# Kernel tuning notes

Measured on AMD Instinct MI355X. Metric: run time of the kernel, lower is better.

Reference implementation:

```python
import jax, jax.numpy as jnp
import numpy as np

N, L, V, IN_DIM, H, E = 128, 128, 8000, 64, 13, 2048
G = 4 * H  # LSTM gate dim (52)

def _lstm_scan(xs, Wih, Whh, b, h0, c0):
    # xs: [L, N, D]; returns final (h, c), each [N, H]
    def step(carry, x_t):
        h, c = carry
        g = x_t @ Wih.T + h @ Whh.T + b
        i, f, gg, o = jnp.split(g, 4, axis=-1)
        c = jax.nn.sigmoid(f) * c + jax.nn.sigmoid(i) * jnp.tanh(gg)
        h = jax.nn.sigmoid(o) * jnp.tanh(c)
        return (h, c), None
    (h, c), _ = jax.lax.scan(step, (h0, c0), xs)
    return h, c

def _gcn_layer(x, W, b, src, dst, norm):
    # GCNConv: out[t] = sum_{(s,t)} norm_st * (x W)[s] + b  (self loops included in src/dst)
    msg = (x @ W)[src] * norm[:, None]
    return jax.ops.segment_sum(msg, dst, num_segments=N) + b

def _gnn(x, params, src, dst, norm):
    W1, b1, W2, b2, Wf, bf = params
    x = jax.nn.leaky_relu(_gcn_layer(x, W1, b1, src, dst, norm), 0.01)
    x = jax.nn.leaky_relu(_gcn_layer(x, W2, b2, src, dst, norm), 0.01)
    return x @ Wf + bf

def setup_inputs():
    ks = iter(jax.random.split(jax.random.key(0), 64))
    def rn(*shape):
        return jax.random.normal(next(ks), shape, dtype=jnp.float32) * 0.1
    inp = {}
    inp["x_tokens"] = jax.random.randint(next(ks), (N, L), 0, V, dtype=jnp.int32)
    inp["edge_index"] = jax.random.randint(next(ks), (2, E), 0, N, dtype=jnp.int32)
    inp["emb"] = rn(V + 1, IN_DIM).at[V].set(0.0)  # padding_idx row zeroed
    for d in ("f", "b"):
        inp["Wih_%s_enc" % d] = rn(G, IN_DIM)
        inp["Whh_%s_enc" % d] = rn(G, H)
        inp["b_%s_enc" % d] = rn(G)
    inp["Wp1"] = rn(2 * H, 2 * H); inp["bp1"] = rn(2 * H)
    inp["Wp2"] = rn(2 * H, 2 * H); inp["bp2"] = rn(2 * H)
    for g in ("gh", "gc"):
        inp[g + "_W1"] = rn(2 * H, 16); inp[g + "_b1"] = rn(16)
        inp[g + "_W2"] = rn(16, 32);    inp[g + "_b2"] = rn(32)
        inp[g + "_Wf"] = rn(32, 2 * H); inp[g + "_bf"] = rn(2 * H)
    for d in ("f", "b"):
        inp["Wih_%s_dec" % d] = rn(G, 1)
        inp["Whh_%s_dec" % d] = rn(G, H)
        inp["b_%s_dec" % d] = rn(G)
    inp["Wout"] = rn(V, 2 * H); inp["bout"] = rn(V)
    return inp

def reference(x_tokens, edge_index, emb, Wih_f_enc, Whh_f_enc, b_f_enc, Wih_b_enc, Whh_b_enc, b_b_enc, Wp1, bp1, Wp2, bp2, gh_W1, gh_b1, gh_W2, gh_b2, gh_Wf, gh_bf, gc_W1, gc_b1, gc_W2, gc_b2, gc_Wf, gc_bf, Wih_f_dec, Whh_f_dec, b_f_dec, Wih_b_dec, Whh_b_dec, b_b_dec, Wout, bout):
    # --- per-node biLSTM encode ---
    xs = jnp.swapaxes(emb[x_tokens], 0, 1)          # [L, N, IN_DIM]
    z = jnp.zeros((N, H), jnp.float32)
    hf, cf = _lstm_scan(xs, Wih_f_enc, Whh_f_enc, b_f_enc, z, z)
    hb, cb = _lstm_scan(xs[::-1], Wih_b_enc, Whh_b_enc, b_b_enc, z, z)
    state_h = jnp.concatenate([hf, hb], -1) @ Wp1.T + bp1   # [N, 2H]
    state_c = jnp.concatenate([cf, cb], -1) @ Wp2.T + bp2
    # --- GCN fusion (symmetric norm with self loops) ---
    ar = jnp.arange(N, dtype=edge_index.dtype)
    src = jnp.concatenate([edge_index[0], ar])
    dst = jnp.concatenate([edge_index[1], ar])
    deg = jax.ops.segment_sum(jnp.ones_like(src, jnp.float32), dst, num_segments=N)
    dinv = jax.lax.rsqrt(jnp.maximum(deg, 1.0))
    norm = dinv[src] * dinv[dst]
    sh = _gnn(state_h, (gh_W1, gh_b1, gh_W2, gh_b2, gh_Wf, gh_bf), src, dst, norm).reshape(N, 2, H)
    sc = _gnn(state_c, (gc_W1, gc_b1, gc_W2, gc_b2, gc_Wf, gc_bf), src, dst, norm).reshape(N, 2, H)
    # --- decoder: each step is a single-timestep biLSTM; original code only
    # passes the GNN state at step 0 and uses a fresh ZERO state for i>0 ---
    prev = jnp.concatenate([jnp.full((N, 1), -1.0, jnp.float32), x_tokens[:, :-1].astype(jnp.float32)], axis=1)  # [N, L]
    first = (jnp.arange(L) == 0)[None, :, None]
    def dec_cell(h0, c0, Wih, Whh, b):
        g = prev[..., None] * Wih[:, 0] + jnp.einsum('nlh,gh->nlg', h0, Whh) + b
        i, f, gg, o = jnp.split(g, 4, axis=-1)
        c = jax.nn.sigmoid(f) * c0 + jax.nn.sigmoid(i) * jnp.tanh(gg)
        return jax.nn.sigmoid(o) * jnp.tanh(c)
    h_f = dec_cell(jnp.where(first, sh[:, 0][:, None, :], 0.0), jnp.where(first, sc[:, 0][:, None, :], 0.0), Wih_f_dec, Whh_f_dec, b_f_dec)
    h_b = dec_cell(jnp.where(first, sh[:, 1][:, None, :], 0.0), jnp.where(first, sc[:, 1][:, None, :], 0.0), Wih_b_dec, Whh_b_dec, b_b_dec)
    dec_out = jnp.concatenate([h_f, h_b], -1)       # [N, L, 2H]
    return jnp.einsum('nld,vd->nlv', dec_out, Wout) + bout   # [N, L, V]
```

## Files before the change

### kernel.cpp

```cpp
#include <hip/hip_runtime.h>
#include <stdint.h>

#define N_    128
#define L_    128
#define V_    8000
#define IN_   64
#define H_    13
#define G_    52
#define E_    2048
#define TWOH  26
#define TOTW  742808

typedef unsigned int   u32;
typedef unsigned short u16;

__device__ __forceinline__ float bfu(u16 u){
    u32 x = ((u32)u) << 16; float f; __builtin_memcpy(&f, &x, 4); return f;
}
__device__ __forceinline__ float sigf(float x){
    x = fminf(fmaxf(x, -30.f), 30.f);
    return 1.0f / (1.0f + __expf(-x));
}
__device__ __forceinline__ float tanh_(float x){
    x = fminf(fmaxf(x, -15.f), 15.f);
    float e = __expf(2.0f * x); return 1.0f - 2.0f / (e + 1.0f);
}

__global__ __launch_bounds__(64) void k_detect(const u16* __restrict__ emb_u16,
                                               int* __restrict__ flag){
    const int lane = threadIdx.x;
    int wild = 0;
    for (int i = lane; i < 1024; i += 64){
        u16 u = emb_u16[i];
        int e = (u >> 7) & 0xFF;
        int tame = (u == 0) || (u == 0x8000) || (e >= 0x60 && e <= 0x88);
        wild += !tame;
    }
    #pragma unroll
    for (int o = 32; o; o >>= 1) wild += __shfl_down(wild, o, 64);
    if (lane == 0) *flag = (wild > 200) ? 1 : 0;
}

struct P31 { const void* p[31]; };

__global__ __launch_bounds__(256) void k_convert(P31 a, const int* __restrict__ flag,
                                                 float* __restrict__ cw){
    const int fp32 = *flag;
    const int i = blockIdx.x * 256 + threadIdx.x;
    if (i >= TOTW) return;
    const int offs[32] = {
        0, 512064, 515392, 516068, 516120, 519448, 520124, 520176, 520852,
        520878, 521554, 521580, 521996, 522012, 522524, 522556, 523388,
        523414, 523830, 523846, 524358, 524390, 525222, 525248, 525300,
        525976, 526028, 526080, 526756, 526808, 734808, TOTW };
    int seg = 0;
    while (i >= offs[seg + 1]) ++seg;
    const int k = i - offs[seg];
    cw[i] = fp32 ? ((const float*)a.p[seg])[k] : bfu(((const u16*)a.p[seg])[k]);
}

__global__ __launch_bounds__(128) void k_proj(const float* __restrict__ emb,
                                              const float* __restrict__ WihF,
                                              const float* __restrict__ WihB,
                                              float* __restrict__ projF,
                                              float* __restrict__ projB){
    __shared__ float x[IN_];
    const int t = blockIdx.x;
    const int tid = threadIdx.x;
    if (tid < IN_) x[tid] = emb[t * IN_ + tid];
    __syncthreads();
    if (tid < 2 * G_){
        const int dir = tid / G_;
        const int g   = tid - dir * G_;
        const float* w = (dir ? WihB : WihF) + g * IN_;
        float acc = 0.f;
        #pragma unroll
        for (int i = 0; i < IN_; ++i) acc += x[i] * w[i];
        (dir ? projB : projF)[t * G_ + g] = acc;
    }
}

__global__ __launch_bounds__(128) void k_lstm(const int* __restrict__ toks_g,
        const float* __restrict__ projF, const float* __restrict__ projB,
        const float* __restrict__ WhhF, const float* __restrict__ bF,
        const float* __restrict__ WhhB, const float* __restrict__ bB,
        const float* __restrict__ Wp1, const float* __restrict__ bp1,
        const float* __restrict__ Wp2, const float* __restrict__ bp2,
        float* __restrict__ state_h, float* __restrict__ state_c){
    __shared__ int   toks[L_];
    __shared__ float hcat[TWOH];
    __shared__ float ccat[TWOH];
    const int n = blockIdx.x, tid = threadIdx.x;
    const int wave = tid >> 6, lane = tid & 63;
    if (tid < L_) toks[tid] = toks_g[n * L_ + tid];

    const float* proj = wave ? projB : projF;
    const float* Whh  = wave ? WhhB : WhhF;
    const float* bp   = wave ? bB   : bF;

    float wh[H_];
    #pragma unroll
    for (int j = 0; j < H_; ++j) wh[j] = 0.f;
    float bb = 0.f;
    if (lane < G_){
        bb = bp[lane];
        #pragma unroll
        for (int j = 0; j < H_; ++j) wh[j] = Whh[lane * H_ + j];
    }
    __syncthreads();

    float h = 0.f, c = 0.f;
    int tok0 = wave ? toks[L_ - 1] : toks[0];
    float gpre = (lane < G_) ? proj[tok0 * G_ + lane] : 0.f;

    for (int t = 0; t < L_; ++t){
        float gv = gpre + bb;
        if (t + 1 < L_){
            int tn = wave ? toks[L_ - 2 - t] : toks[t + 1];
            gpre = (lane < G_) ? proj[tn * G_ + lane] : 0.f;
        }
        #pragma unroll
        for (int j = 0; j < H_; ++j) gv += __shfl(h, j, 64) * wh[j];
        float iv = __shfl(gv, lane,      64);
        float fv = __shfl(gv, lane + 13, 64);
        float gg = __shfl(gv, lane + 26, 64);
        float ov = __shfl(gv, lane + 39, 64);
        c = sigf(fv) * c + sigf(iv) * tanh_(gg);
        h = sigf(ov) * tanh_(c);
    }

    if (lane < H_){ hcat[wave * H_ + lane] = h; ccat[wave * H_ + lane] = c; }
    __syncthreads();

    if (lane < TWOH){
        if (wave == 0){
            float a = bp1[lane];
            #pragma unroll
            for (int k = 0; k < TWOH; ++k) a += hcat[k] * Wp1[lane * TWOH + k];
            state_h[n * TWOH + lane] = a;
        } else {
            float a = bp2[lane];
            #pragma unroll
            for (int k = 0; k < TWOH; ++k) a += ccat[k] * Wp2[lane * TWOH + k];
            state_c[n * TWOH + lane] = a;
        }
    }
}

__global__ __launch_bounds__(256) void k_gcn(const int* __restrict__ eidx,
        const float* __restrict__ state_h, const float* __restrict__ state_c,
        const float* gh_W1, const float* gh_b1, const float* gh_W2, const float* gh_b2,
        const float* gh_Wf, const float* gh_bf,
        const float* gc_W1, const float* gc_b1, const float* gc_W2, const float* gc_b2,
        const float* gc_Wf, const float* gc_bf,
        float* __restrict__ sh, float* __restrict__ sc){
    __shared__ float xs[N_][33];
    __shared__ float xw[N_][33];
    __shared__ float dinv[N_];
    __shared__ int   ptr[N_ + 1];
    __shared__ int   cnt[N_];
    __shared__ int   scn[N_];
    __shared__ int   srcs[E_];
    const int tid = threadIdx.x;
    const int p = blockIdx.x;
    const float* xin = p ? state_c : state_h;
    const float* W1  = p ? gc_W1 : gh_W1;  const float* b1  = p ? gc_b1 : gh_b1;
    const float* W2  = p ? gc_W2 : gh_W2;  const float* b2  = p ? gc_b2 : gh_b2;
    const float* Wf  = p ? gc_Wf : gh_Wf;  const float* bfp = p ? gc_bf : gh_bf;
    float* outp = p ? sc : sh;

    for (int i = tid; i < N_ * TWOH; i += 256) xs[i / TWOH][i % TWOH] = xin[i];
    if (tid < N_) cnt[tid] = 0;
    __syncthreads();
    for (int e = tid; e < E_; e += 256) atomicAdd(&cnt[eidx[E_ + e]], 1);
    __syncthreads();
    if (tid < N_){
        dinv[tid] = rsqrtf((float)cnt[tid] + 1.0f);
        scn[tid]  = cnt[tid];
    }
    __syncthreads();
    for (int off = 1; off < N_; off <<= 1){
        int v = 0;
        if (tid < N_ && tid >= off) v = scn[tid - off];
        __syncthreads();
        if (tid < N_) scn[tid] += v;
        __syncthreads();
    }
    if (tid < N_){
        ptr[tid + 1] = scn[tid];
        if (tid == 0) ptr[0] = 0;
        cnt[tid] = 0;
    }
    __syncthreads();
    for (int e = tid; e < E_; e += 256){
        int d = eidx[E_ + e];
        int pos = atomicAdd(&cnt[d], 1);
        srcs[ptr[d] + pos] = eidx[e];
    }
    __syncthreads();

    for (int i = tid; i < N_ * 16; i += 256){
        int nn = i >> 4, f = i & 15;
        float a = 0.f;
        #pragma unroll
        for (int k = 0; k < TWOH; ++k) a += xs[nn][k] * W1[k * 16 + f];
        xw[nn][f] = a;
    }
    __syncthreads();
    for (int i = tid; i < N_ * 16; i += 256){
        int nn = i >> 4, f = i & 15;
        float dn = dinv[nn];
        float a = dn * dn * xw[nn][f];
        const int e1 = ptr[nn + 1];
        for (int e = ptr[nn]; e < e1; ++e){
            int s = srcs[e];
            a += dn * dinv[s] * xw[s][f];
        }
        a += b1[f];
        xs[nn][f] = a > 0.f ? a : 0.01f * a;
    }
    __syncthreads();

    for (int i = tid; i < N_ * 32; i += 256){
        int nn = i >> 5, f = i & 31;
        float a = 0.f;
        #pragma unroll
        for (int k = 0; k < 16; ++k) a += xs[nn][k] * W2[k * 32 + f];
        xw[nn][f] = a;
    }
    __syncthreads();
    for (int i = tid; i < N_ * 32; i += 256){
        int nn = i >> 5, f = i & 31;
        float dn = dinv[nn];
        float a = dn * dn * xw[nn][f];
        const int e1 = ptr[nn + 1];
        for (int e = ptr[nn]; e < e1; ++e){
            int s = srcs[e];
            a += dn * dinv[s] * xw[s][f];
        }
        a += b2[f];
        xs[nn][f] = a > 0.f ? a : 0.01f * a;
    }
    __syncthreads();

    for (int i = tid; i < N_ * TWOH; i += 256){
        int nn = i / TWOH, d = i % TWOH;
        float a = bfp[d];
        #pragma unroll
        for (int k = 0; k < 32; ++k) a += xs[nn][k] * Wf[k * TWOH + d];
        outp[i] = a;
    }
}

__global__ __launch_bounds__(256) void k_dec(const int* __restrict__ toks,
        const float* __restrict__ sh, const float* __restrict__ sc,
        const float* WihF, const float* WhhF, const float* bF,
        const float* WihB, const float* WhhB, const float* bB,
        float* __restrict__ dec){
    __shared__ float wih[2][G_], bias[2][G_], whh[2][G_][H_];
    const int tid = threadIdx.x;
    for (int i = tid; i < 2 * G_; i += 256){
        int d = i / G_, k = i % G_;
        wih[d][k]  = (d ? WihB : WihF)[k];
        bias[d][k] = (d ? bB : bF)[k];
    }
    for (int i = tid; i < 2 * G_ * H_; i += 256){
        int d = i / (G_ * H_), rr = i % (G_ * H_), k = rr / H_, j = rr % H_;
        whh[d][k][j] = (d ? WhhB : WhhF)[k * H_ + j];
    }
    __syncthreads();

    const int r = blockIdx.x * 256 + tid;
    const int n = r >> 7, l = r & 127;
    const bool first = (l == 0);
    const float prev = first ? -1.0f : (float)toks[n * L_ + l - 1];

    for (int d = 0; d < 2; ++d){
        float h0[H_], c0[H_];
        #pragma unroll
        for (int j = 0; j < H_; ++j){
            h0[j] = first ? sh[n * TWOH + d * H_ + j] : 0.f;
            c0[j] = first ? sc[n * TWOH + d * H_ + j] : 0.f;
        }
        #pragma unroll
        for (int j = 0; j < H_; ++j){
            float gi = prev * wih[d][j]      + bias[d][j];
            float gf = prev * wih[d][13 + j] + bias[d][13 + j];
            float gg = prev * wih[d][26 + j] + bias[d][26 + j];
            float go = prev * wih[d][39 + j] + bias[d][39 + j];
            if (first){
                #pragma unroll
                for (int k = 0; k < H_; ++k){
                    float hk = h0[k];
                    gi += hk * whh[d][j][k];
                    gf += hk * whh[d][13 + j][k];
                    gg += hk * whh[d][26 + j][k];
                    go += hk * whh[d][39 + j][k];
                }
            }
            float cc = sigf(gf) * c0[j] + sigf(gi) * tanh_(gg);
            float hh = sigf(go) * tanh_(cc);
            dec[(size_t)r * TWOH + d * H_ + j] = hh;
        }
    }
}

#define RT 64
#define VT 512
__global__ __launch_bounds__(128) void k_out(const float* __restrict__ dec,
        const float* __restrict__ Wout, const float* __restrict__ bout,
        float* __restrict__ out){
    __shared__ float dl[RT * 28];
    __shared__ float wl[VT * 26];
    const int tid = threadIdx.x;
    const int r0 = blockIdx.x * RT;
    const int v0 = blockIdx.y * VT;
    const int nv = min(VT, V_ - v0);

    for (int i = tid; i < RT * 28; i += 128){
        int rr = i / 28, k = i % 28;
        dl[i] = (k < TWOH) ? dec[(size_t)(r0 + rr) * TWOH + k] : 0.f;
    }
    {
        const float4* src = (const float4*)(Wout + (size_t)v0 * TWOH);
        float4* dst4 = (float4*)wl;
        const int n4 = nv * TWOH / 4;
        for (int i = tid; i < n4; i += 128) dst4[i] = src[i];
    }
    __syncthreads();

    const int lv = 4 * tid;
    if (lv < nv){
        float w[4][28];
        #pragma unroll
        for (int c = 0; c < 4; ++c){
            #pragma unroll
            for (int k = 0; k < TWOH; ++k) w[c][k] = wl[(lv + c) * TWOH + k];
            w[c][26] = 0.f; w[c][27] = 0.f;
        }
        const int v = v0 + lv;
        const float b0 = bout[v],     b1 = bout[v + 1];
        const float b2 = bout[v + 2], b3 = bout[v + 3];
        float4* outp = (float4*)(out + (size_t)r0 * V_ + v);
        #pragma unroll 2
        for (int rr = 0; rr < RT; ++rr){
            float4 d4[7];
            const float4* dp4 = (const float4*)(dl + rr * 28);
            #pragma unroll
            for (int j = 0; j < 7; ++j) d4[j] = dp4[j];
            float s0 = b0, s1 = b1, s2 = b2, s3 = b3;
            const float* dk = (const float*)d4;
            #pragma unroll
            for (int k = 0; k < 28; ++k){
                float dv = dk[k];
                s0 += dv * w[0][k]; s1 += dv * w[1][k];
                s2 += dv * w[2][k]; s3 += dv * w[3][k];
            }
            outp[(size_t)rr * (V_ / 4)] = make_float4(s0, s1, s2, s3);
        }
    }
}

extern "C" void kernel_launch(void* const* d_in, const int* in_sizes, int n_in,
                              void* d_out, int out_size, void* d_ws, size_t ws_size,
                              hipStream_t stream){
    int*   flag  = (int*)d_ws;
    float* cw    = (float*)d_ws + 64;
    float* projF = cw + TOTW;
    float* projB = projF + 416000;
    float* state_h = projB + 416000;
    float* state_c = state_h + 3328;
    float* sh      = state_c + 3328;
    float* sc      = sh + 3328;
    float* dec     = sc + 3328;

    float* cEmb   = cw + 0;
    float* cWihF  = cw + 512064;
    float* cWhhF  = cw + 515392;
    float* cbF    = cw + 516068;
    float* cWihB  = cw + 516120;
    float* cWhhB  = cw + 519448;
    float* cbB    = cw + 520124;
    float* cWp1   = cw + 520176;
    float* cbp1   = cw + 520852;
    float* cWp2   = cw + 520878;
    float* cbp2   = cw + 521554;
    float* cghW1  = cw + 521580;
    float* cghb1  = cw + 521996;
    float* cghW2  = cw + 522012;
    float* cghb2  = cw + 522524;
    float* cghWf  = cw + 522556;
    float* cghbf  = cw + 523388;
    float* cgcW1  = cw + 523414;
    float* cgcb1  = cw + 523830;
    float* cgcW2  = cw + 523846;
    float* cgcb2  = cw + 524358;
    float* cgcWf  = cw + 524390;
    float* cgcbf  = cw + 525222;
    float* cWihFd = cw + 525248;
    float* cWhhFd = cw + 525300;
    float* cbFd   = cw + 525976;
    float* cWihBd = cw + 526028;
    float* cWhhBd = cw + 526080;
    float* cbBd   = cw + 526756;
    float* cWout  = cw + 526808;
    float* cbout  = cw + 734808;

    const int* x_tokens   = (const int*)d_in[0];
    const int* edge_index = (const int*)d_in[1];

    P31 a;
    for (int j = 0; j < 31; ++j) a.p[j] = d_in[2 + j];

    k_detect<<<1, 64, 0, stream>>>((const u16*)d_in[2], flag);
    k_convert<<<(TOTW + 255) / 256, 256, 0, stream>>>(a, flag, cw);
    k_proj<<<V_, 128, 0, stream>>>(cEmb, cWihF, cWihB, projF, projB);
    k_lstm<<<N_, 128, 0, stream>>>(x_tokens, projF, projB,
                                   cWhhF, cbF, cWhhB, cbB,
                                   cWp1, cbp1, cWp2, cbp2, state_h, state_c);
    k_gcn<<<2, 256, 0, stream>>>(edge_index, state_h, state_c,
                                 cghW1, cghb1, cghW2, cghb2, cghWf, cghbf,
                                 cgcW1, cgcb1, cgcW2, cgcb2, cgcWf, cgcbf,
                                 sh, sc);
    k_dec<<<(N_ * L_) / 256, 256, 0, stream>>>(x_tokens, sh, sc,
                                               cWihFd, cWhhFd, cbFd,
                                               cWihBd, cWhhBd, cbBd, dec);
    k_out<<<dim3((N_ * L_) / RT, (V_ + VT - 1) / VT), 128, 0, stream>>>(dec, cWout, cbout, (float*)d_out);
}
```

Measured before the change: 908.7 us.

## Batch embedding projection per block and remap output GEMM to one vocab column per thread

k_proj now handles 8 embedding rows per 256-thread block. It stages both input weight matrices in shared memory, padded to avoid bank conflicts, so weights are reused across rows instead of re-read from global memory per token. k_out changes from 4 vocab columns per thread with float4 stores to 1 column per thread with a 256-wide vocab tile, giving coalesced scalar stores across the wave and fewer registers per thread. The trade-off is more blocks loading the dec tile, and the loss of vectorized per-thread stores.

```diff
diff --git a/kernel.cpp b/kernel.cpp
--- a/kernel.cpp
+++ b/kernel.cpp
@@ -59,24 +59,29 @@
     cw[i] = fp32 ? ((const float*)a.p[seg])[k] : bfu(((const u16*)a.p[seg])[k]);
 }
 
-__global__ __launch_bounds__(128) void k_proj(const float* __restrict__ emb,
+#define TPER 8
+__global__ __launch_bounds__(256) void k_proj(const float* __restrict__ emb,
                                               const float* __restrict__ WihF,
                                               const float* __restrict__ WihB,
                                               float* __restrict__ projF,
                                               float* __restrict__ projB){
-    __shared__ float x[IN_];
-    const int t = blockIdx.x;
+    __shared__ float w[2][G_][IN_ + 1];
+    __shared__ float x[TPER][IN_];
+    const int t0 = blockIdx.x * TPER;
     const int tid = threadIdx.x;
-    if (tid < IN_) x[tid] = emb[t * IN_ + tid];
-    __syncthreads();
-    if (tid < 2 * G_){
-        const int dir = tid / G_;
-        const int g   = tid - dir * G_;
-        const float* w = (dir ? WihB : WihF) + g * IN_;
+    for (int i = tid; i < 2 * G_ * IN_; i += 256){
+        int d = i / (G_ * IN_), r = (i % (G_ * IN_)) / IN_, k = i % IN_;
+        w[d][r][k] = (d ? WihB : WihF)[r * IN_ + k];
+    }
+    for (int i = tid; i < TPER * IN_; i += 256)
+        x[i / IN_][i % IN_] = emb[(size_t)(t0 + i / IN_) * IN_ + i % IN_];
+    __syncthreads();
+    for (int i = tid; i < TPER * 2 * G_; i += 256){
+        const int t = i / (2 * G_), rem = i % (2 * G_), d = rem / G_, g = rem % G_;
         float acc = 0.f;
         #pragma unroll
-        for (int i = 0; i < IN_; ++i) acc += x[i] * w[i];
-        (dir ? projB : projF)[t * G_ + g] = acc;
+        for (int k = 0; k < IN_; ++k) acc += x[t][k] * w[d][g][k];
+        (d ? projB : projF)[(size_t)(t0 + t) * G_ + g] = acc;
     }
 }
 
@@ -306,18 +311,18 @@
 }
 
 #define RT 64
-#define VT 512
-__global__ __launch_bounds__(128) void k_out(const float* __restrict__ dec,
+#define VT 256
+__global__ __launch_bounds__(256) void k_out(const float* __restrict__ dec,
         const float* __restrict__ Wout, const float* __restrict__ bout,
         float* __restrict__ out){
     __shared__ float dl[RT * 28];
-    __shared__ float wl[VT * 26];
+    __shared__ float wl[VT * TWOH];
     const int tid = threadIdx.x;
     const int r0 = blockIdx.x * RT;
     const int v0 = blockIdx.y * VT;
     const int nv = min(VT, V_ - v0);
 
-    for (int i = tid; i < RT * 28; i += 128){
+    for (int i = tid; i < RT * 28; i += 256){
         int rr = i / 28, k = i % 28;
         dl[i] = (k < TWOH) ? dec[(size_t)(r0 + rr) * TWOH + k] : 0.f;
     }
@@ -325,38 +330,31 @@
         const float4* src = (const float4*)(Wout + (size_t)v0 * TWOH);
         float4* dst4 = (float4*)wl;
         const int n4 = nv * TWOH / 4;
-        for (int i = tid; i < n4; i += 128) dst4[i] = src[i];
-    }
-    __syncthreads();
-
-    const int lv = 4 * tid;
-    if (lv < nv){
-        float w[4][28];
-        #pragma unroll
-        for (int c = 0; c < 4; ++c){
-            #pragma unroll
-            for (int k = 0; k < TWOH; ++k) w[c][k] = wl[(lv + c) * TWOH + k];
-            w[c][26] = 0.f; w[c][27] = 0.f;
-        }
-        const int v = v0 + lv;
-        const float b0 = bout[v],     b1 = bout[v + 1];
-        const float b2 = bout[v + 2], b3 = bout[v + 3];
-        float4* outp = (float4*)(out + (size_t)r0 * V_ + v);
-        #pragma unroll 2
+        for (int i = tid; i < n4; i += 256) dst4[i] = src[i];
+    }
+    __syncthreads();
+
+    if (tid < nv){
+        float w[28];
+        #pragma unroll
+        for (int k = 0; k < TWOH; ++k) w[k] = wl[tid * TWOH + k];
+        w[26] = 0.f; w[27] = 0.f;
+        const int v = v0 + tid;
+        const float b0 = bout[v];
+        float* outp = out + (size_t)r0 * V_ + v;
         for (int rr = 0; rr < RT; ++rr){
             float4 d4[7];
             const float4* dp4 = (const float4*)(dl + rr * 28);
             #pragma unroll
             for (int j = 0; j < 7; ++j) d4[j] = dp4[j];
-            float s0 = b0, s1 = b1, s2 = b2, s3 = b3;
             const float* dk = (const float*)d4;
+            float sA = b0, sB = 0.f;
             #pragma unroll
-            for (int k = 0; k < 28; ++k){
-                float dv = dk[k];
-                s0 += dv * w[0][k]; s1 += dv * w[1][k];
-                s2 += dv * w[2][k]; s3 += dv * w[3][k];
+            for (int k = 0; k < 28; k += 2){
+                sA += dk[k]     * w[k];
+                sB += dk[k + 1] * w[k + 1];
             }
-            outp[(size_t)rr * (V_ / 4)] = make_float4(s0, s1, s2, s3);
+            outp[(size_t)rr * V_] = sA + sB;
         }
     }
 }
@@ -414,7 +412,7 @@
 
     k_detect<<<1, 64, 0, stream>>>((const u16*)d_in[2], flag);
     k_convert<<<(TOTW + 255) / 256, 256, 0, stream>>>(a, flag, cw);
-    k_proj<<<V_, 128, 0, stream>>>(cEmb, cWihF, cWihB, projF, projB);
+    k_proj<<<V_ / TPER, 256, 0, stream>>>(cEmb, cWihF, cWihB, projF, projB);
     k_lstm<<<N_, 128, 0, stream>>>(x_tokens, projF, projB,
                                    cWhhF, cbF, cWhhB, cbB,
                                    cWp1, cbp1, cWp2, cbp2, state_h, state_c);
@@ -425,5 +423,5 @@
     k_dec<<<(N_ * L_) / 256, 256, 0, stream>>>(x_tokens, sh, sc,
                                                cWihFd, cWhhFd, cbFd,
                                                cWihBd, cWhhBd, cbBd, dec);
-    k_out<<<dim3((N_ * L_) / RT, (V_ + VT - 1) / VT), 128, 0, stream>>>(dec, cWout, cbout, (float*)d_out);
-}
+    k_out<<<dim3((N_ * L_) / RT, (V_ + VT - 1) / VT), 256, 0, stream>>>(dec, cWout, cbout, (float*)d_out);
+}
```

After: 840.9 us. 1.08x faster.
